# Optimization experiments

Hardware: AMD Instinct MI355X
Metric: run time of the kernel (lower is better)

## Reference

```python
import jax, jax.numpy as jnp
import numpy as np

P = 12           # AR order == number of rollout steps
N = 2048         # input_size (nodes)
B = 128          # batch
C = 1            # channels (only channel 0 used)


def setup_inputs() -> dict:
    key = jax.random.key(0)
    kx, kw = jax.random.split(key)
    x = jax.random.normal(kx, (B, N, C, P), dtype=jnp.float32)
    W = jax.random.normal(kw, (P, N, N), dtype=jnp.float32)
    return {"x": x, "W": W}


def reference(x, W):
    # x: [B, N, C, L]; take channel 0 and transpose -> [B, L(=p), N]
    xt = jnp.transpose(x[:, :, 0, :], (0, 2, 1))

    def step(xc, _):
        # einsum('ijk,bik->bij') followed by sum over i fuses to 'ijk,bik->bj'
        y = jnp.einsum('ijk,bik->bj', W, xc)              # [B, N]
        xc = jnp.concatenate([xc[:, 1:, :], y[:, None, :]], axis=1)  # shift window
        return xc, y

    _, ys = jax.lax.scan(step, xt, None, length=12)       # ys: [12, B, N]
    return jnp.transpose(ys, (1, 2, 0))                   # [B, N, 12]
```

## Files before the change

### kernel.cpp

```cpp
#include <hip/hip_runtime.h>
#include <stdint.h>


typedef _Float16 f16x8 __attribute__((ext_vector_type(8)));
typedef float    f32x4 __attribute__((ext_vector_type(4)));

#define B_ 128
#define N_ 2048
#define P_ 12
#define K_ (P_*N_)
#define KSPLIT 32
#define KCH (K_/KSPLIT)
#define NPHASE (KCH/128)
#define NTILES 16
#define NKP (K_/64)

#define WPK_BYTES   ((size_t)NTILES*NKP*16384)
#define H_SLOT_BYTES ((size_t)B_*N_*2)
#define H_BYTES     (23*H_SLOT_BYTES)
#define PART_BYTES  ((size_t)KSPLIT*B_*N_*2)
#define WS_NEEDED   (WPK_BYTES + H_BYTES + PART_BYTES)

__device__ __constant__ int E_TAB[11] = {7, 13, 18, 24, 29, 35, 40, 46, 51, 57, 62};

__device__ __forceinline__ int e_of_slot(int g) {
    return (g < 12) ? 0 : E_TAB[g - 12];
}
__device__ __forceinline__ float pow2f(int e) {
    return __uint_as_float((uint32_t)(127 + e) << 23);
}

union F16x8 { _Float16 h[8]; uint4 q; };
union F16x4v { _Float16 h[4]; uint2 q; };

__device__ __forceinline__ uint32_t h_off(int slot, int b, int k) {
    return (uint32_t)slot * (uint32_t)H_SLOT_BYTES
         + (uint32_t)(k >> 5) * 8192u + (uint32_t)(((k >> 3) & 3) << 11)
         + (uint32_t)(b << 4) + (uint32_t)((k & 7) << 1);
}

__device__ __forceinline__ size_t w_tile_base(int nt, int pk) {
    return ((size_t)nt * NKP + (size_t)pk) * 16384;
}

__global__ void prep_all(const float* __restrict__ x, const float* __restrict__ W,
                         char* __restrict__ Wp, char* __restrict__ H)
{
    __shared__ float tile[128][68];
    int bid = blockIdx.x, t = threadIdx.x;
    if (bid < 128) {
        int tg = bid * 256 + t;
        int b = tg >> 8;
        int n0 = (tg & 255) << 3;
        const float4* s4 = (const float4*)(x + ((size_t)b * N_ + n0) * P_);
        float4 tmp[24];
        #pragma unroll
        for (int i2 = 0; i2 < 24; ++i2) tmp[i2] = s4[i2];
        #pragma unroll
        for (int p = 0; p < 12; ++p) {
            F16x8 o;
            #pragma unroll
            for (int q = 0; q < 8; ++q) {
                int fi = q * 12 + p;
                float4 blk = tmp[fi >> 2];
                float f = ((fi & 3) == 0) ? blk.x : ((fi & 3) == 1) ? blk.y : ((fi & 3) == 2) ? blk.z : blk.w;
                o.h[q] = (_Float16)f;
            }
            *(uint4*)(H + h_off(p, b, n0)) = o.q;
        }
        return;
    }
    int u = bid - 128;
    int nt = u / NKP, pk = u % NKP;
    int i  = pk >> 5;
    int k0 = (pk & 31) << 6;
    int j0 = nt << 7;
    #pragma unroll
    for (int pass = 0; pass < 8; ++pass) {
        int jl = pass * 16 + (t >> 4);
        int kq = (t & 15) * 4;
        float4 v = *(const float4*)(W + ((size_t)i * N_ + (j0 + jl)) * N_ + k0 + kq);
        tile[jl][kq + 0] = v.x; tile[jl][kq + 1] = v.y;
        tile[jl][kq + 2] = v.z; tile[jl][kq + 3] = v.w;
    }
    __syncthreads();
    int ksub = t >> 7, c = t & 127;
    char* base = Wp + w_tile_base(nt, pk) + (ksub << 13);
    #pragma unroll
    for (int ko = 0; ko < 4; ++ko) {
        F16x8 o;
        #pragma unroll
        for (int q = 0; q < 8; ++q) o.h[q] = (_Float16)tile[c][ksub * 32 + ko * 8 + q];
        uint32_t off = (uint32_t)((c << 6) + (ko << 4)) ^ (uint32_t)((c & 7) << 4);
        *(uint4*)(base + off) = o.q;
    }
}

__global__ __launch_bounds__(256, 2) void gemm_step(
        const char* __restrict__ Wp, const char* __restrict__ H,
        _Float16* __restrict__ partial, int st)
{
    __shared__ alignas(16) char ldsB[2][32768];
    const int tid  = threadIdx.x;
    const int lane = tid & 63;
    const int wv   = tid >> 6;
    const int wr   = wv >> 1;
    const int wc   = wv & 1;
    const int bid  = blockIdx.x;
    const int ks    = bid % KSPLIT;
    const int ntile = bid / KSPLIT;
    const int jbase = (ntile << 7) + (wc << 6) + (lane & 15);
    const int ko   = lane >> 4;
    const int kbase = ks * KCH;
    const int pk0  = kbase >> 6;

    uint32_t boff[4];
    #pragma unroll
    for (int nf = 0; nf < 4; ++nf) {
        int c = (wc << 6) + (nf << 4) + (lane & 15);
        boff[nf] = (uint32_t)((c << 6) + (ko << 4)) ^ (uint32_t)((c & 7) << 4);
    }

    auto stage = [&](int buf, int ph) {
        const char* src = Wp + w_tile_base(ntile, pk0 + (ph << 1));
        #pragma unroll
        for (int j = 0; j < 8; ++j) {
            uint32_t o = (uint32_t)(j << 12) + (uint32_t)(tid << 4);
            __builtin_amdgcn_global_load_lds(
                (const __attribute__((address_space(1))) void*)(src + o),
                (__attribute__((address_space(3))) void*)&ldsB[buf][(j << 12) + (wv << 10)], 16, 0, 0);
        }
    };
    auto loadA = [&](int ph, f16x8 a[4][4]) {
        #pragma unroll
        for (int ksub = 0; ksub < 4; ++ksub) {
            int kg = kbase + (ph << 7) + (ksub << 5);
            const char* sb = H + (size_t)(st + (kg >> 11)) * H_SLOT_BYTES
                           + (uint32_t)(((kg & 2047) >> 5) << 13) + (uint32_t)(ko << 11);
            #pragma unroll
            for (int m = 0; m < 4; ++m) {
                int brow = (wr << 6) + (m << 4) + (lane & 15);
                a[ksub][m] = *(const f16x8*)(sb + (brow << 4));
            }
        }
    };

    f32x4 acc[4][4];
    #pragma unroll
    for (int m = 0; m < 4; ++m)
        #pragma unroll
        for (int n = 0; n < 4; ++n) acc[m][n] = (f32x4){0.f, 0.f, 0.f, 0.f};

    f16x8 a[4][4];
    loadA(0, a);
    stage(0, 0);
    __syncthreads();

    int cur_e = e_of_slot(st + (kbase >> 11));
    #pragma unroll 1
    for (int ph = 0; ph < NPHASE; ++ph) {
        int e_new = e_of_slot(st + ((kbase + (ph << 7)) >> 11));
        if (e_new != cur_e) {
            float f = pow2f(cur_e - e_new);
            #pragma unroll
            for (int m = 0; m < 4; ++m)
                #pragma unroll
                for (int n = 0; n < 4; ++n) acc[m][n] *= f;
            cur_e = e_new;
        }
        if (ph + 1 < NPHASE) stage((ph & 1) ^ 1, ph + 1);
        f16x8 an[4][4];
        if (ph + 1 < NPHASE) loadA(ph + 1, an);
        const char* lb = &ldsB[ph & 1][0];
        #pragma unroll
        for (int ksub = 0; ksub < 4; ++ksub) {
            f16x8 bf[4];
            #pragma unroll
            for (int nf = 0; nf < 4; ++nf)
                bf[nf] = *(const f16x8*)(lb + (ksub << 13) + boff[nf]);
            #pragma unroll
            for (int m = 0; m < 4; ++m)
                #pragma unroll
                for (int nf = 0; nf < 4; ++nf)
                    acc[m][nf] = __builtin_amdgcn_mfma_f32_16x16x32_f16(a[ksub][m], bf[nf], acc[m][nf], 0, 0, 0);
        }
        #pragma unroll
        for (int ksub = 0; ksub < 4; ++ksub)
            #pragma unroll
            for (int m = 0; m < 4; ++m) a[ksub][m] = an[ksub][m];
        __syncthreads();
    }

    const int r0 = (lane >> 4) << 2;
    _Float16* pb = partial + ((size_t)ks * B_ + (wr << 6) + r0) * N_ + jbase;
    #pragma unroll
    for (int m = 0; m < 4; ++m)
        #pragma unroll
        for (int n = 0; n < 4; ++n)
            #pragma unroll
            for (int r = 0; r < 4; ++r)
                pb[(size_t)(m * 16 + r) * N_ + n * 16] = (_Float16)acc[m][n][r];
}

__global__ void reduce_step(const _Float16* __restrict__ partial, float* __restrict__ out,
                            char* __restrict__ H, int t)
{
    int tid = blockIdx.x * 256 + threadIdx.x;
    int b = tid >> 9;
    int n0 = (tid & 511) << 2;
    float s0 = 0.f, s1 = 0.f, s2 = 0.f, s3 = 0.f;
    #pragma unroll 4
    for (int c = 0; c < KSPLIT; ++c) {
        float sc = pow2f(e_of_slot(t + ((c * KCH + (KCH - 64)) >> 11)));
        F16x4v p;
        p.q = *(const uint2*)(partial + ((size_t)c * B_ + b) * N_ + n0);
        s0 += (float)p.h[0] * sc; s1 += (float)p.h[1] * sc;
        s2 += (float)p.h[2] * sc; s3 += (float)p.h[3] * sc;
    }
    float* ob = out + ((size_t)b * N_ + n0) * P_ + t;
    ob[0 * P_] = s0; ob[1 * P_] = s1; ob[2 * P_] = s2; ob[3 * P_] = s3;
    if (t < 11) {
        float ds = pow2f(-E_TAB[t]);
        F16x4v o;
        o.h[0] = (_Float16)(s0 * ds); o.h[1] = (_Float16)(s1 * ds);
        o.h[2] = (_Float16)(s2 * ds); o.h[3] = (_Float16)(s3 * ds);
        *(uint2*)(H + h_off(12 + t, b, n0)) = o.q;
    }
}

__global__ void naive_step(const float* __restrict__ x, const float* __restrict__ W,
                           float* __restrict__ out, int t)
{
    int tid = blockIdx.x * 256 + threadIdx.x;
    int b = tid >> 11;
    int j = tid & (N_ - 1);
    float acc = 0.f;
    for (int i = 0; i < 12; ++i) {
        int g = t + i;
        const float* src = (g < 12) ? (x   + (size_t)b * (N_ * 12) + g)
                                    : (out + (size_t)b * (N_ * 12) + (g - 12));
        const float* wr = W + ((size_t)i * N_ + j) * N_;
        for (int k = 0; k < N_; ++k)
            acc += wr[k] * src[(size_t)k * 12];
    }
    out[((size_t)b * N_ + j) * 12 + t] = acc;
}

extern "C" void kernel_launch(void* const* d_in, const int* in_sizes, int n_in,
                              void* d_out, int out_size, void* d_ws, size_t ws_size,
                              hipStream_t stream)
{
    const float* x = (const float*)d_in[0];
    const float* W = (const float*)d_in[1];
    float* out = (float*)d_out;

    if (ws_size < WS_NEEDED) {
        for (int t = 0; t < 12; ++t)
            naive_step<<<1024, 256, 0, stream>>>(x, W, out, t);
        return;
    }

    char* ws = (char*)d_ws;
    char* Wp = ws;
    char* H  = Wp + WPK_BYTES;
    _Float16* partial = (_Float16*)(H + H_BYTES);

    prep_all<<<6272, 256, 0, stream>>>(x, W, Wp, H);
    for (int t = 0; t < 12; ++t) {
        gemm_step<<<512, 256, 0, stream>>>(Wp, H, partial, t);
        reduce_step<<<256, 256, 0, stream>>>(partial, out, H, t);
    }
}
```

Measured before the change: 539.8 us.

## Precompute all input-only partial products in one launch, then per-step feedback GEMMs

Contributions from the original 12 input slots are now computed once for all future steps in a single large gemm_F launch, which uses a triangular mapping over (step, slot) pairs. Each step then only runs a small gemm_FB over the previously generated feedback slots and reduces the precomputed and feedback partials together. The aim is to replace twelve full-K GEMM launches, each re-reading the whole packed W, with one well-occupied batch plus growing small launches that cover only the dependent part. The cost is extra workspace for 78 plus 44 partial buffers and a changed phase/tile size (64-wide K phases with half-size LDS buffers).

```diff
diff --git a/kernel.cpp b/kernel.cpp
--- a/kernel.cpp
+++ b/kernel.cpp
@@ -9,23 +9,19 @@
 #define N_ 2048
 #define P_ 12
 #define K_ (P_*N_)
-#define KSPLIT 32
-#define KCH (K_/KSPLIT)
-#define NPHASE (KCH/128)
-#define NTILES 16
+#define NT 16
 #define NKP (K_/64)
 
-#define WPK_BYTES   ((size_t)NTILES*NKP*16384)
+#define WPK_BYTES    ((size_t)NT*NKP*16384)
 #define H_SLOT_BYTES ((size_t)B_*N_*2)
-#define H_BYTES     (23*H_SLOT_BYTES)
-#define PART_BYTES  ((size_t)KSPLIT*B_*N_*2)
-#define WS_NEEDED   (WPK_BYTES + H_BYTES + PART_BYTES)
+#define H_BYTES      (23*H_SLOT_BYTES)
+#define CH_BYTES     ((size_t)B_*N_*2)
+#define PF_BYTES     (78*CH_BYTES)
+#define PFB_BYTES    (44*CH_BYTES)
+#define WS_NEEDED    (WPK_BYTES + H_BYTES + PF_BYTES + PFB_BYTES)
 
 __device__ __constant__ int E_TAB[11] = {7, 13, 18, 24, 29, 35, 40, 46, 51, 57, 62};
 
-__device__ __forceinline__ int e_of_slot(int g) {
-    return (g < 12) ? 0 : E_TAB[g - 12];
-}
 __device__ __forceinline__ float pow2f(int e) {
     return __uint_as_float((uint32_t)(127 + e) << 23);
 }
@@ -38,7 +34,6 @@
          + (uint32_t)(k >> 5) * 8192u + (uint32_t)(((k >> 3) & 3) << 11)
          + (uint32_t)(b << 4) + (uint32_t)((k & 7) << 1);
 }
-
 __device__ __forceinline__ size_t w_tile_base(int nt, int pk) {
     return ((size_t)nt * NKP + (size_t)pk) * 16384;
 }
@@ -96,50 +91,46 @@
     }
 }
 
-__global__ __launch_bounds__(256, 2) void gemm_step(
+__device__ __forceinline__ void gemm_body(
         const char* __restrict__ Wp, const char* __restrict__ H,
-        _Float16* __restrict__ partial, int st)
-{
-    __shared__ alignas(16) char ldsB[2][32768];
+        _Float16* __restrict__ part, char* ldsB,
+        int nt, int pk0, int slot, int k0, int nph)
+{
     const int tid  = threadIdx.x;
     const int lane = tid & 63;
     const int wv   = tid >> 6;
     const int wr   = wv >> 1;
     const int wc   = wv & 1;
-    const int bid  = blockIdx.x;
-    const int ks    = bid % KSPLIT;
-    const int ntile = bid / KSPLIT;
-    const int jbase = (ntile << 7) + (wc << 6) + (lane & 15);
+    const int l15  = lane & 15;
     const int ko   = lane >> 4;
-    const int kbase = ks * KCH;
-    const int pk0  = kbase >> 6;
+    const int jbase = (nt << 7) + (wc << 6) + l15;
 
     uint32_t boff[4];
     #pragma unroll
     for (int nf = 0; nf < 4; ++nf) {
-        int c = (wc << 6) + (nf << 4) + (lane & 15);
+        int c = (wc << 6) + (nf << 4) + l15;
         boff[nf] = (uint32_t)((c << 6) + (ko << 4)) ^ (uint32_t)((c & 7) << 4);
     }
 
     auto stage = [&](int buf, int ph) {
-        const char* src = Wp + w_tile_base(ntile, pk0 + (ph << 1));
-        #pragma unroll
-        for (int j = 0; j < 8; ++j) {
+        const char* src = Wp + w_tile_base(nt, pk0 + ph);
+        #pragma unroll
+        for (int j = 0; j < 4; ++j) {
             uint32_t o = (uint32_t)(j << 12) + (uint32_t)(tid << 4);
             __builtin_amdgcn_global_load_lds(
                 (const __attribute__((address_space(1))) void*)(src + o),
-                (__attribute__((address_space(3))) void*)&ldsB[buf][(j << 12) + (wv << 10)], 16, 0, 0);
+                (__attribute__((address_space(3))) void*)(ldsB + buf * 16384 + (j << 12) + (wv << 10)), 16, 0, 0);
         }
     };
-    auto loadA = [&](int ph, f16x8 a[4][4]) {
-        #pragma unroll
-        for (int ksub = 0; ksub < 4; ++ksub) {
-            int kg = kbase + (ph << 7) + (ksub << 5);
-            const char* sb = H + (size_t)(st + (kg >> 11)) * H_SLOT_BYTES
-                           + (uint32_t)(((kg & 2047) >> 5) << 13) + (uint32_t)(ko << 11);
+    auto loadA = [&](int ph, f16x8 a[2][4]) {
+        #pragma unroll
+        for (int ksub = 0; ksub < 2; ++ksub) {
+            int k = k0 + (ph << 6) + (ksub << 5);
+            const char* sb = H + (size_t)slot * H_SLOT_BYTES
+                           + (uint32_t)((k >> 5) << 13) + (uint32_t)(ko << 11);
             #pragma unroll
             for (int m = 0; m < 4; ++m) {
-                int brow = (wr << 6) + (m << 4) + (lane & 15);
+                int brow = (wr << 6) + (m << 4) + l15;
                 a[ksub][m] = *(const f16x8*)(sb + (brow << 4));
             }
         }
@@ -151,48 +142,39 @@
         #pragma unroll
         for (int n = 0; n < 4; ++n) acc[m][n] = (f32x4){0.f, 0.f, 0.f, 0.f};
 
-    f16x8 a[4][4];
+    f16x8 a[2][4];
     loadA(0, a);
     stage(0, 0);
     __syncthreads();
 
-    int cur_e = e_of_slot(st + (kbase >> 11));
     #pragma unroll 1
-    for (int ph = 0; ph < NPHASE; ++ph) {
-        int e_new = e_of_slot(st + ((kbase + (ph << 7)) >> 11));
-        if (e_new != cur_e) {
-            float f = pow2f(cur_e - e_new);
-            #pragma unroll
-            for (int m = 0; m < 4; ++m)
-                #pragma unroll
-                for (int n = 0; n < 4; ++n) acc[m][n] *= f;
-            cur_e = e_new;
-        }
-        if (ph + 1 < NPHASE) stage((ph & 1) ^ 1, ph + 1);
-        f16x8 an[4][4];
-        if (ph + 1 < NPHASE) loadA(ph + 1, an);
-        const char* lb = &ldsB[ph & 1][0];
-        #pragma unroll
-        for (int ksub = 0; ksub < 4; ++ksub) {
-            f16x8 bf[4];
+    for (int ph = 0; ph < nph; ++ph) {
+        if (ph + 1 < nph) stage((ph & 1) ^ 1, ph + 1);
+        const char* lb = ldsB + (ph & 1) * 16384;
+        f16x8 bf[2][4];
+        #pragma unroll
+        for (int ksub = 0; ksub < 2; ++ksub)
             #pragma unroll
             for (int nf = 0; nf < 4; ++nf)
-                bf[nf] = *(const f16x8*)(lb + (ksub << 13) + boff[nf]);
+                bf[ksub][nf] = *(const f16x8*)(lb + (ksub << 13) + boff[nf]);
+        f16x8 an[2][4];
+        if (ph + 1 < nph) loadA(ph + 1, an);
+        #pragma unroll
+        for (int ksub = 0; ksub < 2; ++ksub)
             #pragma unroll
             for (int m = 0; m < 4; ++m)
                 #pragma unroll
                 for (int nf = 0; nf < 4; ++nf)
-                    acc[m][nf] = __builtin_amdgcn_mfma_f32_16x16x32_f16(a[ksub][m], bf[nf], acc[m][nf], 0, 0, 0);
-        }
-        #pragma unroll
-        for (int ksub = 0; ksub < 4; ++ksub)
+                    acc[m][nf] = __builtin_amdgcn_mfma_f32_16x16x32_f16(a[ksub][m], bf[ksub][nf], acc[m][nf], 0, 0, 0);
+        #pragma unroll
+        for (int ksub = 0; ksub < 2; ++ksub)
             #pragma unroll
             for (int m = 0; m < 4; ++m) a[ksub][m] = an[ksub][m];
         __syncthreads();
     }
 
     const int r0 = (lane >> 4) << 2;
-    _Float16* pb = partial + ((size_t)ks * B_ + (wr << 6) + r0) * N_ + jbase;
+    _Float16* pb = part + ((size_t)((wr << 6) + r0)) * N_ + jbase;
     #pragma unroll
     for (int m = 0; m < 4; ++m)
         #pragma unroll
@@ -202,22 +184,62 @@
                 pb[(size_t)(m * 16 + r) * N_ + n * 16] = (_Float16)acc[m][n][r];
 }
 
-__global__ void reduce_step(const _Float16* __restrict__ partial, float* __restrict__ out,
-                            char* __restrict__ H, int t)
+__global__ __launch_bounds__(256, 2) void gemm_F(
+        const char* __restrict__ Wp, const char* __restrict__ H,
+        _Float16* __restrict__ pF)
+{
+    __shared__ alignas(16) char ldsB[2 * 16384];
+    int p = blockIdx.x >> 4, nt = blockIdx.x & 15;
+    int j = 0, t = p;
+    #pragma unroll 1
+    for (int jj = 0; jj < 12; ++jj) {
+        int cnt = 12 - jj;
+        if (t < cnt) { j = jj; break; }
+        t -= cnt;
+    }
+    int idx = t * 12 - t * (t - 1) / 2 + j;
+    gemm_body(Wp, H, pF + (size_t)idx * (CH_BYTES / 2), ldsB,
+              nt, j * 32, t + j, 0, 32);
+}
+
+__global__ __launch_bounds__(256, 2) void gemm_FB(
+        const char* __restrict__ Wp, const char* __restrict__ H,
+        _Float16* __restrict__ pFB, int t)
+{
+    __shared__ alignas(16) char ldsB[2 * 16384];
+    int c = blockIdx.x >> 4, nt = blockIdx.x & 15;
+    int j = c >> 2, sub = c & 3;
+    int i = 12 - t + j;
+    gemm_body(Wp, H, pFB + (size_t)c * (CH_BYTES / 2), ldsB,
+              nt, i * 32 + sub * 8, 12 + j, sub * 512, 8);
+}
+
+__global__ void reduce_step(const _Float16* __restrict__ pF, const _Float16* __restrict__ pFB,
+                            float* __restrict__ out, char* __restrict__ H, int t)
 {
     int tid = blockIdx.x * 256 + threadIdx.x;
     int b = tid >> 9;
     int n0 = (tid & 511) << 2;
+    const size_t eo = (size_t)b * N_ + n0;
     float s0 = 0.f, s1 = 0.f, s2 = 0.f, s3 = 0.f;
+    int baseT = t * 12 - t * (t - 1) / 2;
+    int nF = 12 - t;
     #pragma unroll 4
-    for (int c = 0; c < KSPLIT; ++c) {
-        float sc = pow2f(e_of_slot(t + ((c * KCH + (KCH - 64)) >> 11)));
+    for (int f = 0; f < nF; ++f) {
         F16x4v p;
-        p.q = *(const uint2*)(partial + ((size_t)c * B_ + b) * N_ + n0);
+        p.q = *(const uint2*)(pF + (size_t)(baseT + f) * (CH_BYTES / 2) + eo);
+        s0 += (float)p.h[0]; s1 += (float)p.h[1];
+        s2 += (float)p.h[2]; s3 += (float)p.h[3];
+    }
+    #pragma unroll 4
+    for (int c = 0; c < 4 * t; ++c) {
+        float sc = pow2f(E_TAB[c >> 2]);
+        F16x4v p;
+        p.q = *(const uint2*)(pFB + (size_t)c * (CH_BYTES / 2) + eo);
         s0 += (float)p.h[0] * sc; s1 += (float)p.h[1] * sc;
         s2 += (float)p.h[2] * sc; s3 += (float)p.h[3] * sc;
     }
-    float* ob = out + ((size_t)b * N_ + n0) * P_ + t;
+    float* ob = out + eo * P_ + t;
     ob[0 * P_] = s0; ob[1 * P_] = s1; ob[2 * P_] = s2; ob[3 * P_] = s3;
     if (t < 11) {
         float ds = pow2f(-E_TAB[t]);
@@ -260,14 +282,16 @@
         return;
     }
 
-    char* ws = (char*)d_ws;
-    char* Wp = ws;
+    char* Wp = (char*)d_ws;
     char* H  = Wp + WPK_BYTES;
-    _Float16* partial = (_Float16*)(H + H_BYTES);
+    _Float16* pF  = (_Float16*)(H + H_BYTES);
+    _Float16* pFB = (_Float16*)(H + H_BYTES + PF_BYTES);
 
     prep_all<<<6272, 256, 0, stream>>>(x, W, Wp, H);
-    for (int t = 0; t < 12; ++t) {
-        gemm_step<<<512, 256, 0, stream>>>(Wp, H, partial, t);
-        reduce_step<<<256, 256, 0, stream>>>(partial, out, H, t);
-    }
-}
+    gemm_F<<<1248, 256, 0, stream>>>(Wp, H, pF);
+    reduce_step<<<256, 256, 0, stream>>>(pF, pFB, out, H, 0);
+    for (int t = 1; t < 12; ++t) {
+        gemm_FB<<<64 * t, 256, 0, stream>>>(Wp, H, pFB, t);
+        reduce_step<<<256, 256, 0, stream>>>(pF, pFB, out, H, t);
+    }
+}
```

After: 493.8 us. 1.09x faster.
